# Kernel tuning notes

Hardware: AMD Instinct MI355X
Metric: run time of the kernel (lower is better)

The kernel has to match this reference:

```python
import jax, jax.numpy as jnp
import numpy as np

NUM_EXPERTS = 8
HIDDEN = 1024
INTER = 1024
BATCH = 2
SEQ = 1024
TOP_K = 2
SWIGLU_ALPHA = 1.702
LIMIT = 7.0


def setup_inputs() -> dict:
    key = jax.random.key(0)
    ks = jax.random.split(key, 7)
    hidden_states = jax.random.normal(ks[0], (BATCH, SEQ, HIDDEN), jnp.float32)
    router_indices = jax.random.randint(ks[1], (BATCH * SEQ, TOP_K), 0, NUM_EXPERTS)
    routing_weights = jax.nn.softmax(
        jax.random.normal(ks[2], (BATCH * SEQ, NUM_EXPERTS), jnp.float32), axis=-1)
    scale = 0.02
    gate_up_proj = jax.random.normal(ks[3], (NUM_EXPERTS, HIDDEN, 2 * INTER), jnp.float32) * scale
    gate_up_proj_bias = jax.random.normal(ks[4], (NUM_EXPERTS, 2 * INTER), jnp.float32) * scale
    down_proj = jax.random.normal(ks[5], (NUM_EXPERTS, INTER, HIDDEN), jnp.float32) * scale
    down_proj_bias = jax.random.normal(ks[6], (NUM_EXPERTS, HIDDEN), jnp.float32) * scale
    return {
        "hidden_states": hidden_states,
        "router_indices": router_indices,
        "routing_weights": routing_weights,
        "gate_up_proj": gate_up_proj,
        "gate_up_proj_bias": gate_up_proj_bias,
        "down_proj": down_proj,
        "down_proj_bias": down_proj_bias,
    }


def _grouped_mm(x, w, expert_ids):
    """Grouped GEMM: y[t] = x[t] @ w[expert_ids[t]].

    x: [T, K], w: [E, K, N], expert_ids: [T] int.
    Reference form via one-hot masking (exact equivalent of torch._grouped_mm
    on expert-sorted tokens); guaranteed jit- and grad-safe.
    """
    onehot = jax.nn.one_hot(expert_ids, w.shape[0], dtype=x.dtype)  # [T, E]
    y_all = jnp.einsum('tk,ekn->etn', x, w)                         # [E, T, N]
    return jnp.einsum('te,etn->tn', onehot, y_all)                  # [T, N]


def _gpt_oss_swiglu(x):
    gate = jnp.minimum(x[..., ::2], LIMIT)
    up = jnp.clip(x[..., 1::2], -LIMIT, LIMIT)
    glu = gate * jax.nn.sigmoid(gate * SWIGLU_ALPHA)
    return (up + 1.0) * glu


def reference(hidden_states, router_indices, routing_weights,
              gate_up_proj, gate_up_proj_bias, down_proj, down_proj_bias):
    B = hidden_states.shape[0]
    H = hidden_states.shape[-1]
    x = hidden_states.reshape(-1, H)                       # [M, H]
    M = x.shape[0]
    top_k = router_indices.shape[1]
    num_experts = gate_up_proj.shape[0]

    # routing_weights is [M, num_experts] -> gather the top-k weights
    topk_weights = jnp.take_along_axis(routing_weights, router_indices, axis=1)  # [M, K]

    flat_experts = router_indices.reshape(-1)              # [T = M*K]
    sort_idx = jnp.argsort(flat_experts)                   # expert-sorted order
    sorted_pos = sort_idx // top_k                         # token id per slot
    expert_sorted = flat_experts[sort_idx]                 # [T]
    grouped = x[sorted_pos]                                # [T, H]

    gate_up = _grouped_mm(grouped, gate_up_proj, expert_sorted)
    gate_up = gate_up + gate_up_proj_bias[expert_sorted]   # per-expert bias
    inter = _gpt_oss_swiglu(gate_up)                       # [T, I]

    down = _grouped_mm(inter, down_proj, expert_sorted)
    down = down + down_proj_bias[expert_sorted]            # [T, H]
    down = down * topk_weights.reshape(-1)[sort_idx][:, None]

    out = jnp.zeros((M, H), x.dtype).at[sorted_pos].add(down)  # scatter-add combine
    return out.reshape(B, -1, H)
```

## Files before the change

kernel.cpp:

```cpp
#include <hip/hip_runtime.h>

#define NE 8
#define NH 1024
#define NI 1024
#define NGU 2048
#define MTOK 2048
#define TSLOT 4096

#define MAXT64 80
#define MAXT128 40

typedef short s16x8 __attribute__((ext_vector_type(8)));
typedef float f32x4 __attribute__((ext_vector_type(4)));
typedef unsigned short u16;

#define WS_SEG      0
#define WS_DESC64   64
#define WS_DESC128  384
#define WS_SLOT     1024
#define WS_POS      17408
#define WS_INTER    33792
#define WS_AREG     8422400UL
#define WS_WREG     25199616UL
#define WS_DB_OFF   16777216UL
#define WS_NEED_FAST 58754048UL

__device__ inline u16 f2bf(float f) {
    unsigned u = __builtin_bit_cast(unsigned, f);
    u += 0x7fffu + ((u >> 16) & 1u);
    return (u16)(u >> 16);
}

__device__ inline void lds_dma16(const u16* g, u16* l) {
    __builtin_amdgcn_global_load_lds(
        (const __attribute__((address_space(1))) unsigned int*)g,
        (__attribute__((address_space(3))) unsigned int*)l, 16, 0, 0);
}

__device__ inline int lds_off(int row, int blk) {
    return (row << 7) | (((blk ^ (row & 7)) & 7) << 4);
}

__global__ void k_build(const int* __restrict__ ridx, int* __restrict__ seg,
                        int* __restrict__ d64, int* __restrict__ d128,
                        int* __restrict__ slot_of, int* __restrict__ pos_of) {
    __shared__ int cnt[NE];
    __shared__ int cur[NE];
    int tid = threadIdx.x;
    if (tid < NE) cnt[tid] = 0;
    __syncthreads();
    for (int s = tid; s < TSLOT; s += blockDim.x) atomicAdd(&cnt[ridx[s] & 7], 1);
    __syncthreads();
    if (tid == 0) {
        int a = 0;
        for (int e = 0; e < NE; ++e) { seg[e] = a; cur[e] = a; a += cnt[e]; }
        seg[NE] = a;
        int nt = 0;
        for (int e = 0; e < NE; ++e)
            for (int m0 = 0; m0 < cnt[e]; m0 += 64) d64[nt++] = (e << 16) | (m0 / 64);
        for (; nt < MAXT64; ++nt) d64[nt] = -1;
        nt = 0;
        for (int e = 0; e < NE; ++e)
            for (int m0 = 0; m0 < cnt[e]; m0 += 128) d128[nt++] = (e << 16) | (m0 / 128);
        for (; nt < MAXT128; ++nt) d128[nt] = -1;
    }
    __syncthreads();
    for (int s = tid; s < TSLOT; s += blockDim.x) {
        int e = ridx[s] & 7;
        int p = atomicAdd(&cur[e], 1);
        slot_of[p] = s;
        pos_of[s] = p;
    }
}

__global__ __launch_bounds__(256) void k_gather(const float* __restrict__ x,
                                                const int* __restrict__ slot_of,
                                                u16* __restrict__ A) {
    int r = blockIdx.x;
    int token = slot_of[r] >> 1;
    float4 v = ((const float4*)(x + (size_t)token * NH))[threadIdx.x];
    ushort4 o;
    o.x = f2bf(v.x); o.y = f2bf(v.y); o.z = f2bf(v.z); o.w = f2bf(v.w);
    ((ushort4*)(A + (size_t)r * NH))[threadIdx.x] = o;
}

__global__ __launch_bounds__(256) void k_tr(const float* __restrict__ W,
                                            u16* __restrict__ WT, int K, int N) {
    __shared__ u16 T[64][66];
    int tid = threadIdx.x;
    const float* in = W + (size_t)blockIdx.z * K * N;
    u16* out = WT + (size_t)blockIdx.z * N * K;
    int n0 = blockIdx.x * 64, k0 = blockIdx.y * 64;
#pragma unroll
    for (int p = 0; p < 2; ++p) {
        int kr = p * 32 + (tid >> 4) * 2;
        int nc = (tid & 15) * 4;
        const float* r0 = in + (size_t)(k0 + kr) * N + n0 + nc;
        float4 v0 = *(const float4*)r0;
        float4 v1 = *(const float4*)(r0 + N);
#pragma unroll
        for (int i = 0; i < 4; ++i) {
            unsigned lo = f2bf(((const float*)&v0)[i]);
            unsigned hi = f2bf(((const float*)&v1)[i]);
            *(unsigned*)&T[nc + i][kr] = lo | (hi << 16);
        }
    }
    __syncthreads();
#pragma unroll
    for (int p = 0; p < 2; ++p) {
        int idx = p * 256 + tid;
        int nr = idx >> 3, kc = (idx & 7) * 8;
        unsigned q0 = *(const unsigned*)&T[nr][kc + 0];
        unsigned q1 = *(const unsigned*)&T[nr][kc + 2];
        unsigned q2 = *(const unsigned*)&T[nr][kc + 4];
        unsigned q3 = *(const unsigned*)&T[nr][kc + 6];
        uint4 vv = {q0, q1, q2, q3};
        *(uint4*)(out + (size_t)(n0 + nr) * K + k0 + kc) = vv;
    }
}

__global__ __launch_bounds__(256) void k_gateup_f(
        const u16* __restrict__ A,
        const u16* __restrict__ wt,
        const float* __restrict__ bias,
        const int* __restrict__ seg, const int* __restrict__ desc,
        u16* __restrict__ inter) {
    int d = desc[blockIdx.x];
    if (d < 0) return;
    int e = d >> 16, mt = d & 0xffff;
    int seg0 = seg[e], Te = seg[e + 1] - seg0, m0 = mt * 128;

    __shared__ __align__(16) u16 As[128 * 64];
    __shared__ __align__(16) u16 Bs[64 * 64];

    int tid = threadIdx.x;
    int lane = tid & 63, w = tid >> 6;
    int ml = lane & 15, kq = lane >> 4;
    int wm = w >> 1, wn = w & 1;
    int n0 = blockIdx.y * 64;
    const u16* wte = wt + (size_t)e * NGU * NH;
    int dr = lane >> 3, db = (lane & 7) ^ dr;

    f32x4 zero = {0.f, 0.f, 0.f, 0.f};
    f32x4 acc[4][2];
#pragma unroll
    for (int i = 0; i < 4; ++i) { acc[i][0] = zero; acc[i][1] = zero; }

    for (int kb = 0; kb < NH; kb += 64) {
        __syncthreads();
#pragma unroll
        for (int c = 0; c < 4; ++c) {
            int gr = seg0 + m0 + c * 32 + w * 8 + dr;
            if (gr > TSLOT - 1) gr = TSLOT - 1;
            lds_dma16(A + (size_t)gr * NH + kb + db * 8, As + c * 2048 + w * 512);
        }
#pragma unroll
        for (int c = 0; c < 2; ++c) {
            int row = c * 32 + w * 8 + dr;
            lds_dma16(wte + (size_t)(n0 + row) * NH + kb + db * 8, Bs + c * 2048 + w * 512);
        }
        __syncthreads();

#pragma unroll
        for (int kk = 0; kk < 64; kk += 32) {
            s16x8 af[4], bf[2];
#pragma unroll
            for (int i = 0; i < 4; ++i)
                af[i] = *(const s16x8*)((char*)As + lds_off(wm * 64 + i * 16 + ml, (kk >> 3) + kq));
#pragma unroll
            for (int i = 0; i < 2; ++i)
                bf[i] = *(const s16x8*)((char*)Bs + lds_off(wn * 32 + i * 16 + ml, (kk >> 3) + kq));
#pragma unroll
            for (int mi = 0; mi < 4; ++mi)
#pragma unroll
                for (int ni = 0; ni < 2; ++ni)
                    acc[mi][ni] = __builtin_amdgcn_mfma_f32_16x16x32_bf16(
                        af[mi], bf[ni], acc[mi][ni], 0, 0, 0);
        }
    }

#pragma unroll
    for (int ni = 0; ni < 2; ++ni) {
        int n = n0 + wn * 32 + ni * 16 + ml;
        float bv = bias[e * NGU + n];
#pragma unroll
        for (int mi = 0; mi < 4; ++mi) {
#pragma unroll
            for (int r = 0; r < 4; ++r) {
                float v = acc[mi][ni][r] + bv;
                float pr = __shfl_xor(v, 1, 64);
                float g = (lane & 1) ? pr : v;
                float u = (lane & 1) ? v : pr;
                g = fminf(g, 7.0f);
                u = fminf(fmaxf(u, -7.0f), 7.0f);
                float glu = g / (1.0f + __expf(-1.702f * g));
                float y = (u + 1.0f) * glu;
                int mloc = wm * 64 + mi * 16 + kq * 4 + r;
                if (!(lane & 1) && (m0 + mloc) < Te)
                    inter[(size_t)(seg0 + m0 + mloc) * NI + (n >> 1)] = f2bf(y);
            }
        }
    }
}

__global__ __launch_bounds__(256) void k_down_f(
        const u16* __restrict__ inter,
        const u16* __restrict__ wt,
        const float* __restrict__ bias,
        const int* __restrict__ seg, const int* __restrict__ desc,
        float* __restrict__ dA,
        float* __restrict__ dB) {
    int d = desc[blockIdx.x];
    if (d < 0) return;
    int e = d >> 16, mt = d & 0xffff;
    int seg0 = seg[e], Te = seg[e + 1] - seg0, m0 = mt * 128;
    int kz = blockIdx.z;

    __shared__ __align__(16) u16 As[128 * 64];
    __shared__ __align__(16) u16 Bs[64 * 64];

    int tid = threadIdx.x;
    int lane = tid & 63, w = tid >> 6;
    int ml = lane & 15, kq = lane >> 4;
    int wm = w >> 1, wn = w & 1;
    int n0 = blockIdx.y * 64;
    const u16* wte = wt + (size_t)e * NH * NI;
    int dr = lane >> 3, db = (lane & 7) ^ dr;

    f32x4 zero = {0.f, 0.f, 0.f, 0.f};
    f32x4 acc[4][2];
#pragma unroll
    for (int i = 0; i < 4; ++i) { acc[i][0] = zero; acc[i][1] = zero; }

    int kbeg = kz * (NI / 2);
    for (int kb = kbeg; kb < kbeg + NI / 2; kb += 64) {
        __syncthreads();
#pragma unroll
        for (int c = 0; c < 4; ++c) {
            int gr = seg0 + m0 + c * 32 + w * 8 + dr;
            if (gr > TSLOT - 1) gr = TSLOT - 1;
            lds_dma16(inter + (size_t)gr * NI + kb + db * 8, As + c * 2048 + w * 512);
        }
#pragma unroll
        for (int c = 0; c < 2; ++c) {
            int row = c * 32 + w * 8 + dr;
            lds_dma16(wte + (size_t)(n0 + row) * NI + kb + db * 8, Bs + c * 2048 + w * 512);
        }
        __syncthreads();

#pragma unroll
        for (int kk = 0; kk < 64; kk += 32) {
            s16x8 af[4], bf[2];
#pragma unroll
            for (int i = 0; i < 4; ++i)
                af[i] = *(const s16x8*)((char*)As + lds_off(wm * 64 + i * 16 + ml, (kk >> 3) + kq));
#pragma unroll
            for (int i = 0; i < 2; ++i)
                bf[i] = *(const s16x8*)((char*)Bs + lds_off(wn * 32 + i * 16 + ml, (kk >> 3) + kq));
#pragma unroll
            for (int mi = 0; mi < 4; ++mi)
#pragma unroll
                for (int ni = 0; ni < 2; ++ni)
                    acc[mi][ni] = __builtin_amdgcn_mfma_f32_16x16x32_bf16(
                        af[mi], bf[ni], acc[mi][ni], 0, 0, 0);
        }
    }

    float* dst = kz ? dB : dA;
    float bv[2];
#pragma unroll
    for (int ni = 0; ni < 2; ++ni)
        bv[ni] = (kz == 0) ? bias[e * NH + n0 + wn * 32 + ni * 16 + ml] : 0.0f;

#pragma unroll
    for (int mi = 0; mi < 4; ++mi) {
#pragma unroll
        for (int r = 0; r < 4; ++r) {
            int mloc = wm * 64 + mi * 16 + kq * 4 + r;
            if ((m0 + mloc) < Te) {
                size_t row = (size_t)(seg0 + m0 + mloc);
#pragma unroll
                for (int ni = 0; ni < 2; ++ni) {
                    int n = n0 + wn * 32 + ni * 16 + ml;
                    dst[row * NH + n] = acc[mi][ni][r] + bv[ni];
                }
            }
        }
    }
}

__global__ __launch_bounds__(256) void k_comb(
        const float* __restrict__ dA, const float* __restrict__ dB,
        const float* __restrict__ rw, const int* __restrict__ ridx,
        const int* __restrict__ pos_of, float* __restrict__ out) {
    int t = blockIdx.x;
    int h = threadIdx.x * 4;
    float4 s = {0.f, 0.f, 0.f, 0.f};
#pragma unroll
    for (int k = 0; k < 2; ++k) {
        int slot = t * 2 + k;
        int e = ridx[slot] & 7;
        float wgt = rw[t * NE + e];
        size_t r = (size_t)pos_of[slot];
        float4 a = *(const float4*)(dA + r * NH + h);
        float4 b = *(const float4*)(dB + r * NH + h);
        s.x += wgt * (a.x + b.x);
        s.y += wgt * (a.y + b.y);
        s.z += wgt * (a.z + b.z);
        s.w += wgt * (a.w + b.w);
    }
    *(float4*)(out + (size_t)t * NH + h) = s;
}

__global__ __launch_bounds__(256) void k_gateup_s(
        const float* __restrict__ x, const float* __restrict__ w,
        const float* __restrict__ bias,
        const int* __restrict__ seg, const int* __restrict__ desc,
        const int* __restrict__ slot_of, u16* __restrict__ inter) {
    int d = desc[blockIdx.x];
    if (d < 0) return;
    int e = d >> 16, mt = d & 0xffff;
    int seg0 = seg[e], Te = seg[e + 1] - seg0, m0 = mt * 64;
    __shared__ u16 As[64 * 40];
    __shared__ int tok[64];
    int tid = threadIdx.x;
    if (tid < 64) {
        int m = m0 + tid;
        tok[tid] = (m < Te) ? (slot_of[seg0 + m] >> 1) : -1;
    }
    __syncthreads();
    int lane = tid & 63, wave = tid >> 6;
    int arow = tid >> 2, acol = (tid & 3) * 8;
    int ta = tok[arow];
    int kq = lane >> 4, ml = lane & 15;
    int nb = blockIdx.y * 128 + wave * 32;
    const float* wp = w + (size_t)e * NH * NGU;
    f32x4 zero = {0.f, 0.f, 0.f, 0.f};
    f32x4 acc[4][2];
#pragma unroll
    for (int i = 0; i < 4; ++i) { acc[i][0] = zero; acc[i][1] = zero; }
    for (int kb = 0; kb < NH; kb += 32) {
        float4 a0 = {0, 0, 0, 0}, a1 = {0, 0, 0, 0};
        if (ta >= 0) {
            const float* xp = x + (size_t)ta * NH + kb + acol;
            a0 = *(const float4*)xp; a1 = *(const float4*)(xp + 4);
        }
        s16x8 av;
        av[0] = (short)f2bf(a0.x); av[1] = (short)f2bf(a0.y);
        av[2] = (short)f2bf(a0.z); av[3] = (short)f2bf(a0.w);
        av[4] = (short)f2bf(a1.x); av[5] = (short)f2bf(a1.y);
        av[6] = (short)f2bf(a1.z); av[7] = (short)f2bf(a1.w);
        __syncthreads();
        *(s16x8*)&As[arow * 40 + acol] = av;
        __syncthreads();
        s16x8 afr[4];
#pragma unroll
        for (int msi = 0; msi < 4; ++msi)
            afr[msi] = *(const s16x8*)&As[(msi * 16 + ml) * 40 + kq * 8];
        s16x8 bfr[2];
#pragma unroll
        for (int s = 0; s < 2; ++s) {
            const float* bp = wp + (size_t)(kb + kq * 8) * NGU + nb + s * 16 + ml;
#pragma unroll
            for (int j = 0; j < 8; ++j) bfr[s][j] = (short)f2bf(bp[(size_t)j * NGU]);
        }
#pragma unroll
        for (int msi = 0; msi < 4; ++msi)
#pragma unroll
            for (int s = 0; s < 2; ++s)
                acc[msi][s] = __builtin_amdgcn_mfma_f32_16x16x32_bf16(
                    afr[msi], bfr[s], acc[msi][s], 0, 0, 0);
    }
#pragma unroll
    for (int s = 0; s < 2; ++s) {
        int n = nb + s * 16 + ml;
        float bv = bias[e * NGU + n];
#pragma unroll
        for (int msi = 0; msi < 4; ++msi) {
#pragma unroll
            for (int r = 0; r < 4; ++r) {
                float v = acc[msi][s][r] + bv;
                float pr = __shfl_xor(v, 1, 64);
                float g = (lane & 1) ? pr : v;
                float u = (lane & 1) ? v : pr;
                g = fminf(g, 7.0f);
                u = fminf(fmaxf(u, -7.0f), 7.0f);
                float glu = g / (1.0f + __expf(-1.702f * g));
                float y = (u + 1.0f) * glu;
                int mrow = m0 + msi * 16 + kq * 4 + r;
                if (!(lane & 1) && mrow < Te)
                    inter[(size_t)(seg0 + mrow) * NI + (n >> 1)] = f2bf(y);
            }
        }
    }
}

__global__ __launch_bounds__(256) void k_down_s(
        const u16* __restrict__ inter, const float* __restrict__ w,
        const float* __restrict__ bias, const float* __restrict__ rw,
        const int* __restrict__ seg, const int* __restrict__ desc,
        const int* __restrict__ slot_of, float* __restrict__ out) {
    int d = desc[blockIdx.x];
    if (d < 0) return;
    int e = d >> 16, mt = d & 0xffff;
    int seg0 = seg[e], Te = seg[e + 1] - seg0, m0 = mt * 64;
    __shared__ u16 As[64 * 40];
    int tid = threadIdx.x;
    int lane = tid & 63, wave = tid >> 6;
    int arow = tid >> 2, acol = (tid & 3) * 8;
    bool avalid = (m0 + arow) < Te;
    int kq = lane >> 4, ml = lane & 15;
    int nb = blockIdx.y * 128 + wave * 32;
    const float* wp = w + (size_t)e * NI * NH;
    f32x4 zero = {0.f, 0.f, 0.f, 0.f};
    f32x4 acc[4][2];
#pragma unroll
    for (int i = 0; i < 4; ++i) { acc[i][0] = zero; acc[i][1] = zero; }
    for (int kb = 0; kb < NI; kb += 32) {
        s16x8 av = {0, 0, 0, 0, 0, 0, 0, 0};
        if (avalid) av = *(const s16x8*)(inter + (size_t)(seg0 + m0 + arow) * NI + kb + acol);
        __syncthreads();
        *(s16x8*)&As[arow * 40 + acol] = av;
        __syncthreads();
        s16x8 afr[4];
#pragma unroll
        for (int msi = 0; msi < 4; ++msi)
            afr[msi] = *(const s16x8*)&As[(msi * 16 + ml) * 40 + kq * 8];
        s16x8 bfr[2];
#pragma unroll
        for (int s = 0; s < 2; ++s) {
            const float* bp = wp + (size_t)(kb + kq * 8) * NH + nb + s * 16 + ml;
#pragma unroll
            for (int j = 0; j < 8; ++j) bfr[s][j] = (short)f2bf(bp[(size_t)j * NH]);
        }
#pragma unroll
        for (int msi = 0; msi < 4; ++msi)
#pragma unroll
            for (int s = 0; s < 2; ++s)
                acc[msi][s] = __builtin_amdgcn_mfma_f32_16x16x32_bf16(
                    afr[msi], bfr[s], acc[msi][s], 0, 0, 0);
    }
    float bv[2];
    bv[0] = bias[e * NH + nb + ml];
    bv[1] = bias[e * NH + nb + 16 + ml];
#pragma unroll
    for (int msi = 0; msi < 4; ++msi) {
#pragma unroll
        for (int r = 0; r < 4; ++r) {
            int mrow = m0 + msi * 16 + kq * 4 + r;
            if (mrow < Te) {
                int slot = slot_of[seg0 + mrow];
                int token = slot >> 1;
                float wgt = rw[token * NE + e];
#pragma unroll
                for (int s = 0; s < 2; ++s) {
                    int n = nb + s * 16 + ml;
                    atomicAdd(&out[(size_t)token * NH + n], (acc[msi][s][r] + bv[s]) * wgt);
                }
            }
        }
    }
}

extern "C" void kernel_launch(void* const* d_in, const int* in_sizes, int n_in,
                              void* d_out, int out_size, void* d_ws, size_t ws_size,
                              hipStream_t stream) {
    const float* x   = (const float*)d_in[0];
    const int*   ri  = (const int*)d_in[1];
    const float* rw  = (const float*)d_in[2];
    const float* wgu = (const float*)d_in[3];
    const float* bgu = (const float*)d_in[4];
    const float* wd  = (const float*)d_in[5];
    const float* bd  = (const float*)d_in[6];
    float* out = (float*)d_out;

    char* ws = (char*)d_ws;
    int* seg     = (int*)(ws + WS_SEG);
    int* d64     = (int*)(ws + WS_DESC64);
    int* d128    = (int*)(ws + WS_DESC128);
    int* slot_of = (int*)(ws + WS_SLOT);
    int* pos_of  = (int*)(ws + WS_POS);
    u16* inter   = (u16*)(ws + WS_INTER);

    hipLaunchKernelGGL(k_build, dim3(1), dim3(256), 0, stream, ri, seg, d64, d128,
                       slot_of, pos_of);

    if (ws_size >= WS_NEED_FAST) {
        u16*   aReg = (u16*)(ws + WS_AREG);
        float* dA   = (float*)(ws + WS_AREG);
        u16*   wReg = (u16*)(ws + WS_WREG);
        float* dB   = (float*)(ws + WS_WREG + WS_DB_OFF);

        hipLaunchKernelGGL(k_tr, dim3(NGU / 64, NH / 64, NE), dim3(256), 0, stream,
                           wgu, wReg, NH, NGU);
        hipLaunchKernelGGL(k_gather, dim3(TSLOT), dim3(256), 0, stream, x, slot_of, aReg);
        hipLaunchKernelGGL(k_gateup_f, dim3(MAXT128, NGU / 64), dim3(256), 0, stream,
                           aReg, wReg, bgu, seg, d128, inter);
        hipLaunchKernelGGL(k_tr, dim3(NH / 64, NI / 64, NE), dim3(256), 0, stream,
                           wd, wReg, NI, NH);
        hipLaunchKernelGGL(k_down_f, dim3(MAXT128, NH / 64, 2), dim3(256), 0, stream,
                           inter, wReg, bd, seg, d128, dA, dB);
        hipLaunchKernelGGL(k_comb, dim3(MTOK), dim3(256), 0, stream,
                           dA, dB, rw, ri, pos_of, out);
    } else {
        hipMemsetAsync(out, 0, (size_t)MTOK * NH * sizeof(float), stream);
        hipLaunchKernelGGL(k_gateup_s, dim3(MAXT64, NGU / 128), dim3(256), 0, stream,
                           x, wgu, bgu, seg, d64, slot_of, inter);
        hipLaunchKernelGGL(k_down_s, dim3(MAXT64, NH / 128), dim3(256), 0, stream,
                           inter, wd, bd, rw, seg, d64, slot_of, out);
    }
}
```

Baseline: 238.9 us.

## Drop LDS staging in grouped GEMMs, load MFMA fragments directly from global

Both grouped GEMM kernels stop staging A and B tiles through shared memory with barriers. Each wave now loads its bf16 fragments straight from global memory into registers. The block tile grows to 128x128 with a 64x64 tile per wave, which halves the grid in N. This removes LDS traffic and __syncthreads stalls, but drops the data sharing between waves, so global and L2 traffic rises, and the 16-byte row-strided loads are poorly coalesced.

```diff
diff --git a/kernel.cpp b/kernel.cpp
--- a/kernel.cpp
+++ b/kernel.cpp
@@ -29,16 +29,6 @@
     unsigned u = __builtin_bit_cast(unsigned, f);
     u += 0x7fffu + ((u >> 16) & 1u);
     return (u16)(u >> 16);
-}
-
-__device__ inline void lds_dma16(const u16* g, u16* l) {
-    __builtin_amdgcn_global_load_lds(
-        (const __attribute__((address_space(1))) unsigned int*)g,
-        (__attribute__((address_space(3))) unsigned int*)l, 16, 0, 0);
-}
-
-__device__ inline int lds_off(int row, int blk) {
-    return (row << 7) | (((blk ^ (row & 7)) & 7) << 4);
 }
 
 __global__ void k_build(const int* __restrict__ ridx, int* __restrict__ seg,
@@ -130,58 +120,50 @@
     int e = d >> 16, mt = d & 0xffff;
     int seg0 = seg[e], Te = seg[e + 1] - seg0, m0 = mt * 128;
 
-    __shared__ __align__(16) u16 As[128 * 64];
-    __shared__ __align__(16) u16 Bs[64 * 64];
-
     int tid = threadIdx.x;
     int lane = tid & 63, w = tid >> 6;
     int ml = lane & 15, kq = lane >> 4;
     int wm = w >> 1, wn = w & 1;
-    int n0 = blockIdx.y * 64;
+    int n0 = blockIdx.y * 128 + wn * 64;
     const u16* wte = wt + (size_t)e * NGU * NH;
-    int dr = lane >> 3, db = (lane & 7) ^ dr;
+
+    const u16* pa[4];
+#pragma unroll
+    for (int mi = 0; mi < 4; ++mi) {
+        int row = seg0 + m0 + wm * 64 + mi * 16 + ml;
+        if (row > TSLOT - 1) row = TSLOT - 1;
+        pa[mi] = A + (size_t)row * NH + kq * 8;
+    }
+    const u16* pb[4];
+#pragma unroll
+    for (int ni = 0; ni < 4; ++ni)
+        pb[ni] = wte + (size_t)(n0 + ni * 16 + ml) * NH + kq * 8;
 
     f32x4 zero = {0.f, 0.f, 0.f, 0.f};
-    f32x4 acc[4][2];
-#pragma unroll
-    for (int i = 0; i < 4; ++i) { acc[i][0] = zero; acc[i][1] = zero; }
-
-    for (int kb = 0; kb < NH; kb += 64) {
-        __syncthreads();
-#pragma unroll
-        for (int c = 0; c < 4; ++c) {
-            int gr = seg0 + m0 + c * 32 + w * 8 + dr;
-            if (gr > TSLOT - 1) gr = TSLOT - 1;
-            lds_dma16(A + (size_t)gr * NH + kb + db * 8, As + c * 2048 + w * 512);
-        }
-#pragma unroll
-        for (int c = 0; c < 2; ++c) {
-            int row = c * 32 + w * 8 + dr;
-            lds_dma16(wte + (size_t)(n0 + row) * NH + kb + db * 8, Bs + c * 2048 + w * 512);
-        }
-        __syncthreads();
-
-#pragma unroll
-        for (int kk = 0; kk < 64; kk += 32) {
-            s16x8 af[4], bf[2];
-#pragma unroll
-            for (int i = 0; i < 4; ++i)
-                af[i] = *(const s16x8*)((char*)As + lds_off(wm * 64 + i * 16 + ml, (kk >> 3) + kq));
-#pragma unroll
-            for (int i = 0; i < 2; ++i)
-                bf[i] = *(const s16x8*)((char*)Bs + lds_off(wn * 32 + i * 16 + ml, (kk >> 3) + kq));
-#pragma unroll
-            for (int mi = 0; mi < 4; ++mi)
-#pragma unroll
-                for (int ni = 0; ni < 2; ++ni)
-                    acc[mi][ni] = __builtin_amdgcn_mfma_f32_16x16x32_bf16(
-                        af[mi], bf[ni], acc[mi][ni], 0, 0, 0);
-        }
-    }
-
-#pragma unroll
-    for (int ni = 0; ni < 2; ++ni) {
-        int n = n0 + wn * 32 + ni * 16 + ml;
+    f32x4 acc[4][4];
+#pragma unroll
+    for (int i = 0; i < 4; ++i)
+#pragma unroll
+        for (int j = 0; j < 4; ++j) acc[i][j] = zero;
+
+#pragma unroll 2
+    for (int kb = 0; kb < NH; kb += 32) {
+        s16x8 af[4], bf[4];
+#pragma unroll
+        for (int i = 0; i < 4; ++i) af[i] = *(const s16x8*)(pa[i] + kb);
+#pragma unroll
+        for (int i = 0; i < 4; ++i) bf[i] = *(const s16x8*)(pb[i] + kb);
+#pragma unroll
+        for (int mi = 0; mi < 4; ++mi)
+#pragma unroll
+            for (int ni = 0; ni < 4; ++ni)
+                acc[mi][ni] = __builtin_amdgcn_mfma_f32_16x16x32_bf16(
+                    af[mi], bf[ni], acc[mi][ni], 0, 0, 0);
+    }
+
+#pragma unroll
+    for (int ni = 0; ni < 4; ++ni) {
+        int n = n0 + ni * 16 + ml;
         float bv = bias[e * NGU + n];
 #pragma unroll
         for (int mi = 0; mi < 4; ++mi) {
@@ -216,61 +198,53 @@
     int seg0 = seg[e], Te = seg[e + 1] - seg0, m0 = mt * 128;
     int kz = blockIdx.z;
 
-    __shared__ __align__(16) u16 As[128 * 64];
-    __shared__ __align__(16) u16 Bs[64 * 64];
-
     int tid = threadIdx.x;
     int lane = tid & 63, w = tid >> 6;
     int ml = lane & 15, kq = lane >> 4;
     int wm = w >> 1, wn = w & 1;
-    int n0 = blockIdx.y * 64;
+    int n0 = blockIdx.y * 128 + wn * 64;
     const u16* wte = wt + (size_t)e * NH * NI;
-    int dr = lane >> 3, db = (lane & 7) ^ dr;
+
+    const u16* pa[4];
+#pragma unroll
+    for (int mi = 0; mi < 4; ++mi) {
+        int row = seg0 + m0 + wm * 64 + mi * 16 + ml;
+        if (row > TSLOT - 1) row = TSLOT - 1;
+        pa[mi] = inter + (size_t)row * NI + kq * 8;
+    }
+    const u16* pb[4];
+#pragma unroll
+    for (int ni = 0; ni < 4; ++ni)
+        pb[ni] = wte + (size_t)(n0 + ni * 16 + ml) * NI + kq * 8;
 
     f32x4 zero = {0.f, 0.f, 0.f, 0.f};
-    f32x4 acc[4][2];
-#pragma unroll
-    for (int i = 0; i < 4; ++i) { acc[i][0] = zero; acc[i][1] = zero; }
+    f32x4 acc[4][4];
+#pragma unroll
+    for (int i = 0; i < 4; ++i)
+#pragma unroll
+        for (int j = 0; j < 4; ++j) acc[i][j] = zero;
 
     int kbeg = kz * (NI / 2);
-    for (int kb = kbeg; kb < kbeg + NI / 2; kb += 64) {
-        __syncthreads();
-#pragma unroll
-        for (int c = 0; c < 4; ++c) {
-            int gr = seg0 + m0 + c * 32 + w * 8 + dr;
-            if (gr > TSLOT - 1) gr = TSLOT - 1;
-            lds_dma16(inter + (size_t)gr * NI + kb + db * 8, As + c * 2048 + w * 512);
-        }
-#pragma unroll
-        for (int c = 0; c < 2; ++c) {
-            int row = c * 32 + w * 8 + dr;
-            lds_dma16(wte + (size_t)(n0 + row) * NI + kb + db * 8, Bs + c * 2048 + w * 512);
-        }
-        __syncthreads();
-
-#pragma unroll
-        for (int kk = 0; kk < 64; kk += 32) {
-            s16x8 af[4], bf[2];
-#pragma unroll
-            for (int i = 0; i < 4; ++i)
-                af[i] = *(const s16x8*)((char*)As + lds_off(wm * 64 + i * 16 + ml, (kk >> 3) + kq));
-#pragma unroll
-            for (int i = 0; i < 2; ++i)
-                bf[i] = *(const s16x8*)((char*)Bs + lds_off(wn * 32 + i * 16 + ml, (kk >> 3) + kq));
-#pragma unroll
-            for (int mi = 0; mi < 4; ++mi)
-#pragma unroll
-                for (int ni = 0; ni < 2; ++ni)
-                    acc[mi][ni] = __builtin_amdgcn_mfma_f32_16x16x32_bf16(
-                        af[mi], bf[ni], acc[mi][ni], 0, 0, 0);
-        }
+#pragma unroll 2
+    for (int kb = kbeg; kb < kbeg + NI / 2; kb += 32) {
+        s16x8 af[4], bf[4];
+#pragma unroll
+        for (int i = 0; i < 4; ++i) af[i] = *(const s16x8*)(pa[i] + kb);
+#pragma unroll
+        for (int i = 0; i < 4; ++i) bf[i] = *(const s16x8*)(pb[i] + kb);
+#pragma unroll
+        for (int mi = 0; mi < 4; ++mi)
+#pragma unroll
+            for (int ni = 0; ni < 4; ++ni)
+                acc[mi][ni] = __builtin_amdgcn_mfma_f32_16x16x32_bf16(
+                    af[mi], bf[ni], acc[mi][ni], 0, 0, 0);
     }
 
     float* dst = kz ? dB : dA;
-    float bv[2];
-#pragma unroll
-    for (int ni = 0; ni < 2; ++ni)
-        bv[ni] = (kz == 0) ? bias[e * NH + n0 + wn * 32 + ni * 16 + ml] : 0.0f;
+    float bv[4];
+#pragma unroll
+    for (int ni = 0; ni < 4; ++ni)
+        bv[ni] = (kz == 0) ? bias[e * NH + n0 + ni * 16 + ml] : 0.0f;
 
 #pragma unroll
     for (int mi = 0; mi < 4; ++mi) {
@@ -280,8 +254,8 @@
             if ((m0 + mloc) < Te) {
                 size_t row = (size_t)(seg0 + m0 + mloc);
 #pragma unroll
-                for (int ni = 0; ni < 2; ++ni) {
-                    int n = n0 + wn * 32 + ni * 16 + ml;
+                for (int ni = 0; ni < 4; ++ni) {
+                    int n = n0 + ni * 16 + ml;
                     dst[row * NH + n] = acc[mi][ni][r] + bv[ni];
                 }
             }
@@ -494,11 +468,11 @@
         hipLaunchKernelGGL(k_tr, dim3(NGU / 64, NH / 64, NE), dim3(256), 0, stream,
                            wgu, wReg, NH, NGU);
         hipLaunchKernelGGL(k_gather, dim3(TSLOT), dim3(256), 0, stream, x, slot_of, aReg);
-        hipLaunchKernelGGL(k_gateup_f, dim3(MAXT128, NGU / 64), dim3(256), 0, stream,
+        hipLaunchKernelGGL(k_gateup_f, dim3(MAXT128, NGU / 128), dim3(256), 0, stream,
                            aReg, wReg, bgu, seg, d128, inter);
         hipLaunchKernelGGL(k_tr, dim3(NH / 64, NI / 64, NE), dim3(256), 0, stream,
                            wd, wReg, NI, NH);
-        hipLaunchKernelGGL(k_down_f, dim3(MAXT128, NH / 64, 2), dim3(256), 0, stream,
+        hipLaunchKernelGGL(k_down_f, dim3(MAXT128, NH / 128, 2), dim3(256), 0, stream,
                            inter, wReg, bd, seg, d128, dA, dB);
         hipLaunchKernelGGL(k_comb, dim3(MTOK), dim3(256), 0, stream,
                            dA, dB, rw, ri, pos_of, out);
```

Measured after the change: 337.3 us. 41.2% more time.

## Merge routing build and weight transposes into one prep kernel; fuse gather into gate-up

Applied to the files above, without the earlier changes.

The single-block routing build and both weight transpose/convert kernels become one grid-partitioned prep kernel, so the serial routing build overlaps the transposes and two launches disappear. The separate token gather/bf16 conversion kernel is removed. The gate-up GEMM now reads fp32 hidden rows through a per-tile token table and converts them to bf16 in registers before storing into swizzled LDS. In exchange, each N-block re-reads fp32 activations at twice the bf16 byte count, and the A operand uses plain register loads instead of asynchronous LDS DMA. The fallback path now also runs the prep kernel, which writes full transposed weights into the intermediate region of a possibly small workspace.

```diff
diff --git a/kernel.cpp b/kernel.cpp
--- a/kernel.cpp
+++ b/kernel.cpp
@@ -20,8 +20,8 @@
 #define WS_SLOT     1024
 #define WS_POS      17408
 #define WS_INTER    33792
-#define WS_AREG     8422400UL
-#define WS_WREG     25199616UL
+#define WS_WTD      8422400UL
+#define WS_WTGU     25199616UL
 #define WS_DB_OFF   16777216UL
 #define WS_NEED_FAST 58754048UL
 
@@ -41,56 +41,8 @@
     return (row << 7) | (((blk ^ (row & 7)) & 7) << 4);
 }
 
-__global__ void k_build(const int* __restrict__ ridx, int* __restrict__ seg,
-                        int* __restrict__ d64, int* __restrict__ d128,
-                        int* __restrict__ slot_of, int* __restrict__ pos_of) {
-    __shared__ int cnt[NE];
-    __shared__ int cur[NE];
-    int tid = threadIdx.x;
-    if (tid < NE) cnt[tid] = 0;
-    __syncthreads();
-    for (int s = tid; s < TSLOT; s += blockDim.x) atomicAdd(&cnt[ridx[s] & 7], 1);
-    __syncthreads();
-    if (tid == 0) {
-        int a = 0;
-        for (int e = 0; e < NE; ++e) { seg[e] = a; cur[e] = a; a += cnt[e]; }
-        seg[NE] = a;
-        int nt = 0;
-        for (int e = 0; e < NE; ++e)
-            for (int m0 = 0; m0 < cnt[e]; m0 += 64) d64[nt++] = (e << 16) | (m0 / 64);
-        for (; nt < MAXT64; ++nt) d64[nt] = -1;
-        nt = 0;
-        for (int e = 0; e < NE; ++e)
-            for (int m0 = 0; m0 < cnt[e]; m0 += 128) d128[nt++] = (e << 16) | (m0 / 128);
-        for (; nt < MAXT128; ++nt) d128[nt] = -1;
-    }
-    __syncthreads();
-    for (int s = tid; s < TSLOT; s += blockDim.x) {
-        int e = ridx[s] & 7;
-        int p = atomicAdd(&cur[e], 1);
-        slot_of[p] = s;
-        pos_of[s] = p;
-    }
-}
-
-__global__ __launch_bounds__(256) void k_gather(const float* __restrict__ x,
-                                                const int* __restrict__ slot_of,
-                                                u16* __restrict__ A) {
-    int r = blockIdx.x;
-    int token = slot_of[r] >> 1;
-    float4 v = ((const float4*)(x + (size_t)token * NH))[threadIdx.x];
-    ushort4 o;
-    o.x = f2bf(v.x); o.y = f2bf(v.y); o.z = f2bf(v.z); o.w = f2bf(v.w);
-    ((ushort4*)(A + (size_t)r * NH))[threadIdx.x] = o;
-}
-
-__global__ __launch_bounds__(256) void k_tr(const float* __restrict__ W,
-                                            u16* __restrict__ WT, int K, int N) {
-    __shared__ u16 T[64][66];
-    int tid = threadIdx.x;
-    const float* in = W + (size_t)blockIdx.z * K * N;
-    u16* out = WT + (size_t)blockIdx.z * N * K;
-    int n0 = blockIdx.x * 64, k0 = blockIdx.y * 64;
+__device__ void tr_tile(const float* in, u16* out, int K, int N, int n0, int k0,
+                        u16 T[64][66], int tid) {
 #pragma unroll
     for (int p = 0; p < 2; ++p) {
         int kr = p * 32 + (tid >> 4) * 2;
@@ -119,11 +71,61 @@
     }
 }
 
+__global__ __launch_bounds__(256) void k_prep(
+        const float* __restrict__ wgu, const float* __restrict__ wd,
+        const int* __restrict__ ridx,
+        u16* __restrict__ wtgu, u16* __restrict__ wtd,
+        int* __restrict__ seg, int* __restrict__ d64, int* __restrict__ d128,
+        int* __restrict__ slot_of, int* __restrict__ pos_of) {
+    __shared__ u16 T[64][66];
+    __shared__ int cnt[NE];
+    __shared__ int cur[NE];
+    int bx = blockIdx.x, tid = threadIdx.x;
+    if (bx < 4096) {
+        int e = bx >> 9, rem = bx & 511;
+        int n0 = (rem & 31) * 64, k0 = (rem >> 5) * 64;
+        tr_tile(wgu + (size_t)e * NH * NGU, wtgu + (size_t)e * NGU * NH,
+                NH, NGU, n0, k0, T, tid);
+    } else if (bx < 6144) {
+        int idx = bx - 4096;
+        int e = idx >> 8, rem = idx & 255;
+        int n0 = (rem & 15) * 64, k0 = (rem >> 4) * 64;
+        tr_tile(wd + (size_t)e * NI * NH, wtd + (size_t)e * NH * NI,
+                NI, NH, n0, k0, T, tid);
+    } else {
+        if (tid < NE) cnt[tid] = 0;
+        __syncthreads();
+        for (int s = tid; s < TSLOT; s += blockDim.x) atomicAdd(&cnt[ridx[s] & 7], 1);
+        __syncthreads();
+        if (tid == 0) {
+            int a = 0;
+            for (int e = 0; e < NE; ++e) { seg[e] = a; cur[e] = a; a += cnt[e]; }
+            seg[NE] = a;
+            int nt = 0;
+            for (int e = 0; e < NE; ++e)
+                for (int m0 = 0; m0 < cnt[e]; m0 += 64) d64[nt++] = (e << 16) | (m0 / 64);
+            for (; nt < MAXT64; ++nt) d64[nt] = -1;
+            nt = 0;
+            for (int e = 0; e < NE; ++e)
+                for (int m0 = 0; m0 < cnt[e]; m0 += 128) d128[nt++] = (e << 16) | (m0 / 128);
+            for (; nt < MAXT128; ++nt) d128[nt] = -1;
+        }
+        __syncthreads();
+        for (int s = tid; s < TSLOT; s += blockDim.x) {
+            int e = ridx[s] & 7;
+            int p = atomicAdd(&cur[e], 1);
+            slot_of[p] = s;
+            pos_of[s] = p;
+        }
+    }
+}
+
 __global__ __launch_bounds__(256) void k_gateup_f(
-        const u16* __restrict__ A,
+        const float* __restrict__ x,
         const u16* __restrict__ wt,
         const float* __restrict__ bias,
         const int* __restrict__ seg, const int* __restrict__ desc,
+        const int* __restrict__ slot_of,
         u16* __restrict__ inter) {
     int d = desc[blockIdx.x];
     if (d < 0) return;
@@ -132,28 +134,50 @@
 
     __shared__ __align__(16) u16 As[128 * 64];
     __shared__ __align__(16) u16 Bs[64 * 64];
+    __shared__ int tok[128];
 
     int tid = threadIdx.x;
+    if (tid < 128) {
+        int m = m0 + tid;
+        tok[tid] = (m < Te) ? (slot_of[seg0 + m] >> 1) : -1;
+    }
     int lane = tid & 63, w = tid >> 6;
     int ml = lane & 15, kq = lane >> 4;
     int wm = w >> 1, wn = w & 1;
     int n0 = blockIdx.y * 64;
     const u16* wte = wt + (size_t)e * NGU * NH;
     int dr = lane >> 3, db = (lane & 7) ^ dr;
+    int ar = tid >> 1, ah = tid & 1;
 
     f32x4 zero = {0.f, 0.f, 0.f, 0.f};
     f32x4 acc[4][2];
 #pragma unroll
     for (int i = 0; i < 4; ++i) { acc[i][0] = zero; acc[i][1] = zero; }
 
+    __syncthreads();
+    int ta = tok[ar];
+    const float* xrow = x + (size_t)(ta < 0 ? 0 : ta) * NH + ah * 32;
+
     for (int kb = 0; kb < NH; kb += 64) {
-        __syncthreads();
-#pragma unroll
-        for (int c = 0; c < 4; ++c) {
-            int gr = seg0 + m0 + c * 32 + w * 8 + dr;
-            if (gr > TSLOT - 1) gr = TSLOT - 1;
-            lds_dma16(A + (size_t)gr * NH + kb + db * 8, As + c * 2048 + w * 512);
-        }
+        s16x8 blk[4];
+#pragma unroll
+        for (int j = 0; j < 4; ++j) {
+            float4 u = {0, 0, 0, 0}, v = {0, 0, 0, 0};
+            if (ta >= 0) {
+                u = *(const float4*)(xrow + kb + j * 8);
+                v = *(const float4*)(xrow + kb + j * 8 + 4);
+            }
+            s16x8 t;
+            t[0] = (short)f2bf(u.x); t[1] = (short)f2bf(u.y);
+            t[2] = (short)f2bf(u.z); t[3] = (short)f2bf(u.w);
+            t[4] = (short)f2bf(v.x); t[5] = (short)f2bf(v.y);
+            t[6] = (short)f2bf(v.z); t[7] = (short)f2bf(v.w);
+            blk[j] = t;
+        }
+        __syncthreads();
+#pragma unroll
+        for (int j = 0; j < 4; ++j)
+            *(s16x8*)((char*)As + lds_off(ar, ah * 4 + j)) = blk[j];
 #pragma unroll
         for (int c = 0; c < 2; ++c) {
             int row = c * 32 + w * 8 + dr;
@@ -482,28 +506,25 @@
     int* pos_of  = (int*)(ws + WS_POS);
     u16* inter   = (u16*)(ws + WS_INTER);
 
-    hipLaunchKernelGGL(k_build, dim3(1), dim3(256), 0, stream, ri, seg, d64, d128,
-                       slot_of, pos_of);
-
     if (ws_size >= WS_NEED_FAST) {
-        u16*   aReg = (u16*)(ws + WS_AREG);
-        float* dA   = (float*)(ws + WS_AREG);
-        u16*   wReg = (u16*)(ws + WS_WREG);
-        float* dB   = (float*)(ws + WS_WREG + WS_DB_OFF);
-
-        hipLaunchKernelGGL(k_tr, dim3(NGU / 64, NH / 64, NE), dim3(256), 0, stream,
-                           wgu, wReg, NH, NGU);
-        hipLaunchKernelGGL(k_gather, dim3(TSLOT), dim3(256), 0, stream, x, slot_of, aReg);
+        u16*   wtd  = (u16*)(ws + WS_WTD);
+        u16*   wtgu = (u16*)(ws + WS_WTGU);
+        float* dA   = (float*)(ws + WS_WTGU);
+        float* dB   = (float*)(ws + WS_WTGU + WS_DB_OFF);
+
+        hipLaunchKernelGGL(k_prep, dim3(6145), dim3(256), 0, stream,
+                           wgu, wd, ri, wtgu, wtd, seg, d64, d128, slot_of, pos_of);
         hipLaunchKernelGGL(k_gateup_f, dim3(MAXT128, NGU / 64), dim3(256), 0, stream,
-                           aReg, wReg, bgu, seg, d128, inter);
-        hipLaunchKernelGGL(k_tr, dim3(NH / 64, NI / 64, NE), dim3(256), 0, stream,
-                           wd, wReg, NI, NH);
+                           x, wtgu, bgu, seg, d128, slot_of, inter);
         hipLaunchKernelGGL(k_down_f, dim3(MAXT128, NH / 64, 2), dim3(256), 0, stream,
-                           inter, wReg, bd, seg, d128, dA, dB);
+                           inter, wtd, bd, seg, d128, dA, dB);
         hipLaunchKernelGGL(k_comb, dim3(MTOK), dim3(256), 0, stream,
                            dA, dB, rw, ri, pos_of, out);
     } else {
         hipMemsetAsync(out, 0, (size_t)MTOK * NH * sizeof(float), stream);
+        hipLaunchKernelGGL(k_prep, dim3(6145), dim3(256), 0, stream,
+                           wgu, wd, ri, (u16*)(ws + WS_INTER), (u16*)(ws + WS_INTER),
+                           seg, d64, d128, slot_of, pos_of);
         hipLaunchKernelGGL(k_gateup_s, dim3(MAXT64, NGU / 128), dim3(256), 0, stream,
                            x, wgu, bgu, seg, d64, slot_of, inter);
         hipLaunchKernelGGL(k_down_s, dim3(MAXT64, NH / 128), dim3(256), 0, stream,
```

Result: slower. 287.8 us (+20.5%).
